# Performance work log

Measured on AMD Instinct MI355X. Metric: run time of the kernel, lower is better.

## Reference

```python
import jax, jax.numpy as jnp
import numpy as np

B, T, C = 2, 2048, 1024
N_HEAD, N_GROUP = 16, 4
N_KV = N_HEAD // N_GROUP          # 4
HEAD_DIM = C // N_HEAD            # 64
ROPE_BASE = 10000.0
INIT_STD = 0.02


def setup_inputs() -> dict:
    key = jax.random.key(0)
    ks = jax.random.split(key, 5)
    kvC = N_KV * HEAD_DIM
    return {
        "x": jax.random.normal(ks[0], (B, T, C), jnp.float32),
        "w_q": jax.random.normal(ks[1], (C, C), jnp.float32) * INIT_STD,
        "b_q": jnp.zeros((C,), jnp.float32),
        "w_k": jax.random.normal(ks[2], (C, kvC), jnp.float32) * INIT_STD,
        "b_k": jnp.zeros((kvC,), jnp.float32),
        "w_v": jax.random.normal(ks[3], (C, kvC), jnp.float32) * INIT_STD,
        "b_v": jnp.zeros((kvC,), jnp.float32),
        "w_o": jax.random.normal(ks[4], (C, C), jnp.float32) * INIT_STD,
        "b_o": jnp.zeros((C,), jnp.float32),
    }


def reference(x, w_q, b_q, w_k, b_k, w_v, b_v, w_o, b_o):
    Bx, Tx, Cx = x.shape
    # projections (torch Linear math with weights stored as [in, out])
    q = (x @ w_q + b_q).reshape(Bx, Tx, N_HEAD, HEAD_DIM).transpose(0, 2, 1, 3)  # [B,H,T,hd]
    k = (x @ w_k + b_k).reshape(Bx, Tx, N_KV, HEAD_DIM).transpose(0, 2, 1, 3)    # [B,KV,T,hd]
    v = (x @ w_v + b_v).reshape(Bx, Tx, N_KV, HEAD_DIM).transpose(0, 2, 1, 3)

    # RoPE with INTERLEAVED pair convention: pairs are (dim 2i, dim 2i+1)
    inv_freq = 1.0 / (ROPE_BASE ** (jnp.arange(0, HEAD_DIM, 2, dtype=jnp.float32) / HEAD_DIM))
    freqs = jnp.arange(Tx, dtype=jnp.float32)[:, None] * inv_freq[None, :]       # [T, hd/2]
    cos, sin = jnp.cos(freqs), jnp.sin(freqs)

    def rope(t):
        tp = t.reshape(*t.shape[:-1], HEAD_DIM // 2, 2)
        e, o = tp[..., 0], tp[..., 1]          # even/odd lanes, [B,h,T,hd/2]
        er = e * cos - o * sin
        orr = e * sin + o * cos
        return jnp.stack([er, orr], axis=-1).reshape(t.shape)

    q, k = rope(q), rope(k)

    # GQA: duplicate each KV head n_group times (consecutively, like repeat_interleave)
    k = jnp.repeat(k, N_GROUP, axis=1)   # [B,H,T,hd]
    v = jnp.repeat(v, N_GROUP, axis=1)

    attn = jnp.einsum('bhqd,bhkd->bhqk', q, k) / np.sqrt(HEAD_DIM).astype(np.float32)
    causal = jnp.tril(jnp.ones((Tx, Tx), bool))
    attn = jnp.where(causal, attn, -jnp.inf)
    attn = jax.nn.softmax(attn, axis=-1)

    out = jnp.einsum('bhqk,bhkd->bhqd', attn, v)            # [B,H,T,hd]
    out = out.transpose(0, 2, 1, 3).reshape(Bx, Tx, Cx)
    return out @ w_o + b_o
```

## Files before the change

kernel.cpp:

```cpp
#include <hip/hip_runtime.h>
#include <hip/hip_bf16.h>

typedef __hip_bfloat16 bf16;
typedef __attribute__((ext_vector_type(8))) short short8_t;
typedef __attribute__((ext_vector_type(4))) short short4_t;
typedef __attribute__((ext_vector_type(4))) float f32x4;

#define B_SZ   2
#define T_SEQ  2048
#define C_DIM  1024
#define NH     16
#define NKV    4
#define HD     64
#define QKVW   1536
#define MTOK   (B_SZ * T_SEQ)

#define LOG2_BASE_OVER_32 0.4152410118609203f
#define Q_SCALE 0.1803368801111204f

__device__ __forceinline__ short f2bs(float f) {
    unsigned u = __float_as_uint(f);
    u += 0x7FFFu + ((u >> 16) & 1u);
    return (short)(u >> 16);
}
__device__ __forceinline__ short f2bs_trunc(float f) {
    return (short)(__float_as_uint(f) >> 16);
}
__device__ __forceinline__ float bs2f(short s) {
    unsigned u = ((unsigned)(unsigned short)s) << 16;
    return __uint_as_float(u);
}
__device__ __forceinline__ float dpp_xor1(float x) {
    return __int_as_float(
        __builtin_amdgcn_update_dpp(0, __float_as_int(x), 0xB1, 0xF, 0xF, true));
}
__device__ __forceinline__ float fast_exp2(float x) {
    float r;
    asm("v_exp_f32 %0, %1" : "=v"(r) : "v"(x));
    return r;
}
__device__ __forceinline__ unsigned pack_bf16_trunc(float lo, float hi) {
    return __builtin_amdgcn_perm(__float_as_uint(hi), __float_as_uint(lo),
                                 0x07060302u);
}
__device__ __forceinline__ void gload_lds16(const short* g, short* l) {
    __builtin_amdgcn_global_load_lds(
        (const __attribute__((address_space(1))) void*)g,
        (__attribute__((address_space(3))) void*)l, 16, 0, 0);
}

__device__ __forceinline__ void transpose_tile(
    const float* __restrict__ W, short* __restrict__ Wt,
    int K, int N, int n0, int k0, int tid)
{
    __shared__ float tile[32][33];
    int tx = tid & 31, ty = tid >> 5;
    #pragma unroll
    for (int i = 0; i < 4; ++i)
        tile[ty + 8 * i][tx] = W[(size_t)(k0 + ty + 8 * i) * N + n0 + tx];
    __syncthreads();
    #pragma unroll
    for (int i = 0; i < 4; ++i)
        Wt[(size_t)(n0 + ty + 8 * i) * K + k0 + tx] = f2bs(tile[tx][ty + 8 * i]);
}

__global__ __launch_bounds__(256) void prep_kernel(
    const float* __restrict__ x,
    const float* __restrict__ w_q, const float* __restrict__ w_k,
    const float* __restrict__ w_v, const float* __restrict__ w_o,
    const float* __restrict__ b_q, const float* __restrict__ b_k,
    const float* __restrict__ b_v,
    short* __restrict__ Xb, short* __restrict__ Wqkv, short* __restrict__ Wto,
    float* __restrict__ Bqkv, float2* __restrict__ Tab)
{
    int blk = blockIdx.x, tid = threadIdx.x;
    if (blk < 4096) {
        int i = blk * 1024 + tid * 4;
        float4 v = *(const float4*)(x + i);
        short4_t o;
        o[0] = f2bs(v.x); o[1] = f2bs(v.y); o[2] = f2bs(v.z); o[3] = f2bs(v.w);
        *(short4_t*)(Xb + i) = o;
    } else if (blk < 5120) {
        int l = blk - 4096;
        transpose_tile(w_q, Wqkv, C_DIM, C_DIM, (l & 31) * 32, (l >> 5) * 32, tid);
    } else if (blk < 5376) {
        int l = blk - 5120;
        transpose_tile(w_k, Wqkv + (size_t)1024 * C_DIM, C_DIM, 256,
                       (l & 7) * 32, (l >> 3) * 32, tid);
    } else if (blk < 5632) {
        int l = blk - 5376;
        transpose_tile(w_v, Wqkv + (size_t)1280 * C_DIM, C_DIM, 256,
                       (l & 7) * 32, (l >> 3) * 32, tid);
    } else if (blk < 6656) {
        int l = blk - 5632;
        transpose_tile(w_o, Wto, C_DIM, C_DIM, (l & 31) * 32, (l >> 5) * 32, tid);
    } else if (blk < 6662) {
        int i = (blk - 6656) * 256 + tid;
        float v;
        if (i < 1024)      v = b_q[i];
        else if (i < 1280) v = b_k[i - 1024];
        else               v = b_v[i - 1280];
        Bqkv[i] = v;
    } else {
        int idx = (blk - 6662) * 256 + tid;
        int t = idx >> 5, i = idx & 31;
        float ang = (float)t * exp2f(-(float)i * LOG2_BASE_OVER_32);
        Tab[idx] = make_float2(cosf(ang), sinf(ang));
    }
}

#define GEMM_STAGE(dstA, dstB, Aptr, Bptr, k0)                                  \
    {                                                                           \
        _Pragma("unroll")                                                       \
        for (int it = 0; it < 4; ++it) {                                        \
            int i = (w * 4 + it) * 64 + lane;                                   \
            int row = i >> 3, p = i & 7;                                        \
            int gc = (k0) + ((p ^ (row & 7)) << 3);                             \
            gload_lds16((Aptr) + (size_t)(m0 + row) * K + gc,                   \
                        (dstA) + (w * 4 + it) * 512);                           \
        }                                                                       \
        _Pragma("unroll")                                                       \
        for (int it = 0; it < 4; ++it) {                                        \
            int i = (w * 4 + it) * 64 + lane;                                   \
            int row = i >> 3, p = i & 7;                                        \
            int gc = (k0) + ((p ^ (row & 7)) << 3);                             \
            gload_lds16((Bptr) + (size_t)(n0 + row) * K + gc,                   \
                        (dstB) + (w * 4 + it) * 512);                           \
        }                                                                       \
    }

#define GEMM_COMPUTE(srcA, srcB)                                                \
    {                                                                           \
        _Pragma("unroll")                                                       \
        for (int ks = 0; ks < 2; ++ks) {                                        \
            short8_t af[4], bf[4];                                              \
            _Pragma("unroll")                                                   \
            for (int mt = 0; mt < 4; ++mt) {                                    \
                int r = wm * 64 + mt * 16 + l16;                                \
                int g = ks * 4 + quad;                                          \
                af[mt] = *(const short8_t*)&(srcA)[r * 64 + ((g ^ (r & 7)) << 3)]; \
            }                                                                   \
            _Pragma("unroll")                                                   \
            for (int nt = 0; nt < 4; ++nt) {                                    \
                int r = wn * 64 + nt * 16 + l16;                                \
                int g = ks * 4 + quad;                                          \
                bf[nt] = *(const short8_t*)&(srcB)[r * 64 + ((g ^ (r & 7)) << 3)]; \
            }                                                                   \
            _Pragma("unroll")                                                   \
            for (int mt = 0; mt < 4; ++mt)                                      \
                _Pragma("unroll")                                               \
                for (int nt = 0; nt < 4; ++nt)                                  \
                    acc[mt][nt] = __builtin_amdgcn_mfma_f32_16x16x32_bf16(      \
                        af[mt], bf[nt], acc[mt][nt], 0, 0, 0);                  \
        }                                                                       \
    }

#define GEMM_KLOOP(Aptr, Bptr)                                                  \
    GEMM_STAGE(sA(0), sB(0), Aptr, Bptr, 0);                                    \
    for (int t = 0; t < NT; ++t) {                                              \
        int cur = t & 1;                                                        \
        if (t + 1 < NT) {                                                       \
            GEMM_STAGE(sA(cur ^ 1), sB(cur ^ 1), Aptr, Bptr, (t + 1) * 64);     \
            asm volatile("s_waitcnt vmcnt(8)" ::: "memory");                    \
        } else {                                                                \
            asm volatile("s_waitcnt vmcnt(0)" ::: "memory");                    \
        }                                                                       \
        __builtin_amdgcn_s_barrier();                                           \
        __builtin_amdgcn_sched_barrier(0);                                      \
        GEMM_COMPUTE(sA(cur), sB(cur));                                         \
        __builtin_amdgcn_sched_barrier(0);                                      \
        __builtin_amdgcn_s_barrier();                                           \
    }

__global__ __launch_bounds__(256) void gemm_qkv(
    const short* __restrict__ A, const short* __restrict__ Bt,
    const float* __restrict__ bias, const float2* __restrict__ Tab,
    short* __restrict__ QKVb, short* __restrict__ Vt)
{
    __shared__ __align__(16) short smem[32768];
    #define sA(b) (smem + (b) * 16384)
    #define sB(b) (smem + (b) * 16384 + 8192)

    const int K = C_DIM, NT = C_DIM / 64;
    int bid = blockIdx.x;
    int swz = (bid & 7) * 48 + (bid >> 3);
    int m0 = (swz / 12) * 128;
    int n0 = (swz % 12) * 128;
    int tid  = threadIdx.x;
    int w    = tid >> 6, lane = tid & 63;
    int quad = lane >> 4, l16 = lane & 15;
    int wm = w & 1, wn = w >> 1;

    f32x4 acc[4][4] = {};

    GEMM_KLOOP(A, Bt);

    if (n0 < 1280) {
        float scale = (n0 < 1024) ? Q_SCALE : 1.0f;
        float sgn   = (l16 & 1) ? 1.0f : -1.0f;
        #pragma unroll
        for (int nt = 0; nt < 4; ++nt) {
            int col = n0 + wn * 64 + nt * 16 + l16;
            int ip  = (col & 63) >> 1;
            float bv = bias[col];
            #pragma unroll
            for (int mt = 0; mt < 4; ++mt) {
                #pragma unroll
                for (int r = 0; r < 4; ++r) {
                    int row = m0 + wm * 64 + mt * 16 + quad * 4 + r;
                    float v = acc[mt][nt][r] + bv;
                    float po = dpp_xor1(v);
                    float2 cs = Tab[(row & (T_SEQ - 1)) * 32 + ip];
                    float res = (v * cs.x + sgn * po * cs.y) * scale;
                    QKVb[(size_t)row * QKVW + col] = f2bs(res);
                }
            }
        }
    } else {
        short (*sT)[136] = (short(*)[136])smem;
        #pragma unroll
        for (int h2 = 0; h2 < 2; ++h2) {
            if (wn == h2) {
                #pragma unroll
                for (int nt = 0; nt < 4; ++nt) {
                    int col_l = nt * 16 + l16;
                    float bv = bias[n0 + h2 * 64 + col_l];
                    #pragma unroll
                    for (int mt = 0; mt < 4; ++mt)
                        #pragma unroll
                        for (int r = 0; r < 4; ++r)
                            sT[col_l][wm * 64 + mt * 16 + quad * 4 + r] =
                                f2bs(acc[mt][nt][r] + bv);
                }
            }
            __syncthreads();
            int d0 = n0 - 1280 + h2 * 64;
            #pragma unroll
            for (int it = 0; it < 4; ++it) {
                int slot = tid + 256 * it;
                int dl = slot >> 4, seg = (slot & 15) * 8;
                *(short8_t*)(Vt + (size_t)(d0 + dl) * MTOK + m0 + seg) =
                    *(const short8_t*)&sT[dl][seg];
            }
            __syncthreads();
        }
    }
    #undef sA
    #undef sB
}

__global__ __launch_bounds__(256) void gemm_mfma_o(
    const short* __restrict__ A, const short* __restrict__ Bt,
    const float* __restrict__ bias, float* __restrict__ C,
    int M, int N, int K_, int unused)
{
    __shared__ __align__(16) short smem[32768];
    #define sA(b) (smem + (b) * 16384)
    #define sB(b) (smem + (b) * 16384 + 8192)

    const int K = C_DIM, NT = C_DIM / 64;
    int bid = blockIdx.x;
    int swz = (bid & 7) * 32 + (bid >> 3);
    int m0 = (swz >> 3) * 128;
    int n0 = (swz & 7) * 128;
    int tid  = threadIdx.x;
    int w    = tid >> 6, lane = tid & 63;
    int quad = lane >> 4, l16 = lane & 15;
    int wm = w & 1, wn = w >> 1;

    f32x4 acc[4][4] = {};

    GEMM_KLOOP(A, Bt);

    #pragma unroll
    for (int mt = 0; mt < 4; ++mt) {
        #pragma unroll
        for (int nt = 0; nt < 4; ++nt) {
            int col = n0 + wn * 64 + nt * 16 + l16;
            float bv = bias[col];
            #pragma unroll
            for (int r = 0; r < 4; ++r) {
                int row = m0 + wm * 64 + mt * 16 + quad * 4 + r;
                C[(size_t)row * N + col] = acc[mt][nt][r] + bv;
            }
        }
    }
    #undef sA
    #undef sB
}

__global__ __launch_bounds__(512) void attn_mfma18(
    const short* __restrict__ QKV, const short* __restrict__ Vt,
    short* __restrict__ O)
{
    __shared__ __align__(16) short sK3[3][64][64];
    __shared__ __align__(16) short sVt[2][64][72];

    const int tid  = threadIdx.x;
    const int w    = tid >> 6;
    const int lane = tid & 63;
    const int quad = lane >> 4;
    const int l16  = lane & 15;

    int blk = blockIdx.x;
    int grp = blk & 7;
    int half = blk >> 8;
    int idx8 = (blk & 255) >> 3;
    int pr   = half ? idx8 : 63 - idx8;
    int kvh = grp & 3;
    int b   = grp >> 2;
    int h   = kvh * 4 + (w & 3);
    int tq  = pr * 2 + (w >> 2);
    int ct  = pr >> 1;
    int tg  = tq * 16 + l16;

    const short* qptr = QKV + ((size_t)(b * T_SEQ) + tq * 16 + l16) * QKVW + h * HD;
    short8_t qf0 = *(const short8_t*)(qptr + quad * 8);
    short8_t qf1 = *(const short8_t*)(qptr + quad * 8 + 32);

    const short* kbase  = QKV + (size_t)b * T_SEQ * QKVW + 1024 + kvh * HD;
    const short* vtbase = Vt + (size_t)(kvh * HD) * MTOK + b * T_SEQ;

    float m_l = -INFINITY, l_l = 0.f;
    f32x4 oacc[4];
    #pragma unroll
    for (int dt = 0; dt < 4; ++dt) oacc[dt] = (f32x4){0.f, 0.f, 0.f, 0.f};

    const int kr_  = tid >> 3;
    const int kg   = tid & 7;
    const int ksrc = (kg ^ (kr_ & 7)) << 3;

    const int vdim = tid >> 3;
    const int s8   = tid & 7;
    const int vseg = s8 * 8;
    const int P0   = ((s8 & 4) << 3) | ((s8 & 1) << 4) | ((s8 & 2) << 1);

    const int c0g = quad ^ (l16 & 7);

    short8_t v0 = *(const short8_t*)(vtbase + (size_t)vdim * MTOK + vseg);
    gload_lds16(kbase + (size_t)kr_ * QKVW + ksrc, (short*)sK3[0] + (w << 9));
    if (ct >= 1)
        gload_lds16(kbase + (size_t)(64 + kr_) * QKVW + ksrc,
                    (short*)sK3[1] + (w << 9));
    if (ct >= 2)
        gload_lds16(kbase + (size_t)(128 + kr_) * QKVW + ksrc,
                    (short*)sK3[2] + (w << 9));
    {
        union { short8_t v; short4_t h[2]; } u; u.v = v0;
        *(short4_t*)&sVt[0][vdim][P0]     = u.h[0];
        *(short4_t*)&sVt[0][vdim][P0 + 8] = u.h[1];
    }
    short8_t vr;
    if (ct > 0)
        vr = *(const short8_t*)(vtbase + (size_t)vdim * MTOK + 64 + vseg);
    if (ct >= 2)      asm volatile("s_waitcnt vmcnt(3) lgkmcnt(0)" ::: "memory");
    else if (ct == 1) asm volatile("s_waitcnt vmcnt(2) lgkmcnt(0)" ::: "memory");
    else              asm volatile("s_waitcnt vmcnt(0) lgkmcnt(0)" ::: "memory");
    __builtin_amdgcn_s_barrier();
    __builtin_amdgcn_sched_barrier(0);

    f32x4 sacc[4], sacc_n[4];
    #pragma unroll
    for (int kt = 0; kt < 4; ++kt) {
        f32x4 z = {0.f, 0.f, 0.f, 0.f};
        const short* krow = &sK3[0][l16 + 16 * kt][0];
        short8_t kf0 = *(const short8_t*)(krow + (c0g << 3));
        short8_t kf1 = *(const short8_t*)(krow + ((c0g ^ 4) << 3));
        z = __builtin_amdgcn_mfma_f32_16x16x32_bf16(kf0, qf0, z, 0, 0, 0);
        z = __builtin_amdgcn_mfma_f32_16x16x32_bf16(kf1, qf1, z, 0, 0, 0);
        sacc[kt] = z;
    }

    int kc = 0;
    for (int c = 0; c <= ct; ++c) {
        const int buf = c & 1;
        const int kn  = (kc == 2) ? 0 : kc + 1;

        if (c + 2 <= ct)      asm volatile("s_waitcnt vmcnt(2) lgkmcnt(0)" ::: "memory");
        else if (c + 1 <= ct) asm volatile("s_waitcnt vmcnt(1) lgkmcnt(0)" ::: "memory");
        else                  asm volatile("s_waitcnt lgkmcnt(0)" ::: "memory");
        __builtin_amdgcn_s_barrier();
        __builtin_amdgcn_sched_barrier(0);

        __builtin_amdgcn_s_setprio(1);
        if (c < ct) {
            #pragma unroll
            for (int kt = 0; kt < 4; ++kt) {
                f32x4 z = {0.f, 0.f, 0.f, 0.f};
                const short* krow = &sK3[kn][l16 + 16 * kt][0];
                short8_t kf0 = *(const short8_t*)(krow + (c0g << 3));
                short8_t kf1 = *(const short8_t*)(krow + ((c0g ^ 4) << 3));
                z = __builtin_amdgcn_mfma_f32_16x16x32_bf16(kf0, qf0, z, 0, 0, 0);
                z = __builtin_amdgcn_mfma_f32_16x16x32_bf16(kf1, qf1, z, 0, 0, 0);
                sacc_n[kt] = z;
            }
            if (c + 3 <= ct) {
                int jn = (c + 3) * 64;
                gload_lds16(kbase + (size_t)(jn + kr_) * QKVW + ksrc,
                            (short*)sK3[kc] + (w << 9));
            }
        }

        if (c == ct) {
            int j0 = c * 64;
            #pragma unroll
            for (int kt = 0; kt < 4; ++kt)
                #pragma unroll
                for (int r = 0; r < 4; ++r)
                    if (j0 + 16 * kt + quad * 4 + r > tg) sacc[kt][r] = -INFINITY;
        }

        float v0s = fmaxf(fmaxf(sacc[0][0], sacc[0][1]), fmaxf(sacc[0][2], sacc[0][3]));
        float v1s = fmaxf(fmaxf(sacc[1][0], sacc[1][1]), fmaxf(sacc[1][2], sacc[1][3]));
        float v2s = fmaxf(fmaxf(sacc[2][0], sacc[2][1]), fmaxf(sacc[2][2], sacc[2][3]));
        float v3s = fmaxf(fmaxf(sacc[3][0], sacc[3][1]), fmaxf(sacc[3][2], sacc[3][3]));
        float vloc = fmaxf(fmaxf(v0s, v1s), fmaxf(v2s, v3s));

        if (!__all(vloc <= m_l + 8.0f)) {
            float vmax = fmaxf(vloc, __shfl_xor(vloc, 16));
            vmax = fmaxf(vmax, __shfl_xor(vmax, 32));
            float mnew = fmaxf(m_l, vmax);
            float al = fast_exp2(m_l - mnew);
            m_l = mnew;
            l_l *= al;
            #pragma unroll
            for (int r = 0; r < 4; ++r) {
                float alr = __shfl(al, quad * 4 + r);
                #pragma unroll
                for (int dt = 0; dt < 4; ++dt) oacc[dt][r] *= alr;
            }
        }

        float psum = 0.f;
        unsigned pk0, pk1, pk2, pk3, pk4, pk5, pk6, pk7;
        {
            float p0 = fast_exp2(sacc[0][0] - m_l), p1 = fast_exp2(sacc[0][1] - m_l);
            float p2 = fast_exp2(sacc[0][2] - m_l), p3 = fast_exp2(sacc[0][3] - m_l);
            psum += (p0 + p1) + (p2 + p3);
            pk0 = pack_bf16_trunc(p0, p1); pk1 = pack_bf16_trunc(p2, p3);
        }
        {
            float p0 = fast_exp2(sacc[1][0] - m_l), p1 = fast_exp2(sacc[1][1] - m_l);
            float p2 = fast_exp2(sacc[1][2] - m_l), p3 = fast_exp2(sacc[1][3] - m_l);
            psum += (p0 + p1) + (p2 + p3);
            pk2 = pack_bf16_trunc(p0, p1); pk3 = pack_bf16_trunc(p2, p3);
        }
        {
            float p0 = fast_exp2(sacc[2][0] - m_l), p1 = fast_exp2(sacc[2][1] - m_l);
            float p2 = fast_exp2(sacc[2][2] - m_l), p3 = fast_exp2(sacc[2][3] - m_l);
            psum += (p0 + p1) + (p2 + p3);
            pk4 = pack_bf16_trunc(p0, p1); pk5 = pack_bf16_trunc(p2, p3);
        }
        {
            float p0 = fast_exp2(sacc[3][0] - m_l), p1 = fast_exp2(sacc[3][1] - m_l);
            float p2 = fast_exp2(sacc[3][2] - m_l), p3 = fast_exp2(sacc[3][3] - m_l);
            psum += (p0 + p1) + (p2 + p3);
            pk6 = pack_bf16_trunc(p0, p1); pk7 = pack_bf16_trunc(p2, p3);
        }
        l_l += psum;

        short8_t pf0, pf1;
        {
            union { unsigned u[4]; short8_t v; } fa, fb;
            fa.u[0] = pk0; fa.u[1] = pk1; fa.u[2] = pk2; fa.u[3] = pk3;
            fb.u[0] = pk4; fb.u[1] = pk5; fb.u[2] = pk6; fb.u[3] = pk7;
            pf0 = fa.v; pf1 = fb.v;
        }

        if (c < ct) {
            union { short8_t v; short4_t hh[2]; } u; u.v = vr;
            *(short4_t*)&sVt[buf ^ 1][vdim][P0]     = u.hh[0];
            *(short4_t*)&sVt[buf ^ 1][vdim][P0 + 8] = u.hh[1];
            if (c + 2 <= ct)
                vr = *(const short8_t*)(vtbase + (size_t)vdim * MTOK
                                        + (c + 2) * 64 + vseg);
        }

        #pragma unroll
        for (int dt = 0; dt < 4; ++dt) {
            short8_t vf0 = *(const short8_t*)&sVt[buf][16 * dt + l16][quad * 8];
            short8_t vf1 = *(const short8_t*)&sVt[buf][16 * dt + l16][quad * 8 + 32];
            oacc[dt] = __builtin_amdgcn_mfma_f32_16x16x32_bf16(pf0, vf0, oacc[dt], 0, 0, 0);
            oacc[dt] = __builtin_amdgcn_mfma_f32_16x16x32_bf16(pf1, vf1, oacc[dt], 0, 0, 0);
        }
        __builtin_amdgcn_s_setprio(0);

        #pragma unroll
        for (int kt = 0; kt < 4; ++kt) sacc[kt] = sacc_n[kt];
        kc = kn;
    }

    l_l += __shfl_xor(l_l, 16);
    l_l += __shfl_xor(l_l, 32);

    #pragma unroll
    for (int r = 0; r < 4; ++r) {
        int m = quad * 4 + r;
        float lr = __shfl(l_l, quad * 4 + r);
        float inv = __builtin_amdgcn_rcpf(lr);
        #pragma unroll
        for (int dt = 0; dt < 4; ++dt)
            O[((size_t)b * T_SEQ + tq * 16 + m) * C_DIM + h * HD + 16 * dt + l16] =
                f2bs(oacc[dt][r] * inv);
    }
}

extern "C" void kernel_launch(void* const* d_in, const int* in_sizes, int n_in,
                              void* d_out, int out_size, void* d_ws, size_t ws_size,
                              hipStream_t stream)
{
    const float* x   = (const float*)d_in[0];
    const float* w_q = (const float*)d_in[1];
    const float* b_q = (const float*)d_in[2];
    const float* w_k = (const float*)d_in[3];
    const float* b_k = (const float*)d_in[4];
    const float* w_v = (const float*)d_in[5];
    const float* b_v = (const float*)d_in[6];
    const float* w_o = (const float*)d_in[7];
    const float* b_o = (const float*)d_in[8];
    float* out = (float*)d_out;

    char* ws = (char*)d_ws;
    short*  Xb   = (short*) (ws);
    short*  Ab   = (short*) (ws + ((size_t)8  << 20));
    short*  QKVb = (short*) (ws + ((size_t)16 << 20));
    short*  Wqkv = (short*) (ws + ((size_t)28 << 20));
    short*  Wto  = (short*) (ws + ((size_t)31 << 20));
    float*  Bqkv = (float*) (ws + ((size_t)33 << 20));
    float2* Tab  = (float2*)(ws + ((size_t)33 << 20) + 8192);
    short*  Vt   = (short*) (ws + ((size_t)34 << 20));

    const int M = MTOK;

    prep_kernel<<<6918, 256, 0, stream>>>(
        x, w_q, w_k, w_v, w_o, b_q, b_k, b_v, Xb, Wqkv, Wto, Bqkv, Tab);

    gemm_qkv<<<384, 256, 0, stream>>>(
        Xb, Wqkv, Bqkv, Tab, QKVb, Vt);

    attn_mfma18<<<B_SZ * NKV * 64, 512, 0, stream>>>(QKVb, Vt, Ab);

    gemm_mfma_o<<<256, 256, 0, stream>>>(
        Ab, Wto, b_o, out, M, C_DIM, C_DIM, 0);
}
```

Before: 155.2 us.

## Process two query tiles per wave in attention to reuse K/V fragments

Each attention block now covers a 64-query tile instead of 32. Every wave holds two 16-row query tiles, so each K and V fragment read from LDS feeds two MFMAs, and the grid halves to 256 blocks. The aim is to cut K/V global and LDS traffic per query and to interleave independent MFMA chains. The cost is roughly double the accumulator and score registers. Fewer blocks also means less parallelism and coarser causal load balancing, since the previous paired-tile ordering was replaced by a simple reverse order.

```diff
diff --git a/kernel.cpp b/kernel.cpp
--- a/kernel.cpp
+++ b/kernel.cpp
@@ -289,7 +289,7 @@
     #undef sB
 }
 
-__global__ __launch_bounds__(512) void attn_mfma18(
+__global__ __launch_bounds__(512) void attn_mfma19(
     const short* __restrict__ QKV, const short* __restrict__ Vt,
     short* __restrict__ O)
 {
@@ -304,27 +304,35 @@
 
     int blk = blockIdx.x;
     int grp = blk & 7;
-    int half = blk >> 8;
-    int idx8 = (blk & 255) >> 3;
-    int pr   = half ? idx8 : 63 - idx8;
+    int p   = 31 - (blk >> 3);
     int kvh = grp & 3;
     int b   = grp >> 2;
     int h   = kvh * 4 + (w & 3);
-    int tq  = pr * 2 + (w >> 2);
-    int ct  = pr >> 1;
-    int tg  = tq * 16 + l16;
-
-    const short* qptr = QKV + ((size_t)(b * T_SEQ) + tq * 16 + l16) * QKVW + h * HD;
-    short8_t qf0 = *(const short8_t*)(qptr + quad * 8);
-    short8_t qf1 = *(const short8_t*)(qptr + quad * 8 + 32);
+    int ht  = w >> 2;
+    int tqA = p * 4 + ht * 2;
+    int tqB = tqA + 1;
+    int ct  = p;
+    int tgA = tqA * 16 + l16;
+    int tgB = tqB * 16 + l16;
+
+    const short* qpA = QKV + ((size_t)(b * T_SEQ) + tqA * 16 + l16) * QKVW + h * HD;
+    const short* qpB = QKV + ((size_t)(b * T_SEQ) + tqB * 16 + l16) * QKVW + h * HD;
+    short8_t qf0a = *(const short8_t*)(qpA + quad * 8);
+    short8_t qf1a = *(const short8_t*)(qpA + quad * 8 + 32);
+    short8_t qf0b = *(const short8_t*)(qpB + quad * 8);
+    short8_t qf1b = *(const short8_t*)(qpB + quad * 8 + 32);
 
     const short* kbase  = QKV + (size_t)b * T_SEQ * QKVW + 1024 + kvh * HD;
     const short* vtbase = Vt + (size_t)(kvh * HD) * MTOK + b * T_SEQ;
 
-    float m_l = -INFINITY, l_l = 0.f;
-    f32x4 oacc[4];
+    float m_a = -INFINITY, l_a = 0.f;
+    float m_b = -INFINITY, l_b = 0.f;
+    f32x4 oaccA[4], oaccB[4];
     #pragma unroll
-    for (int dt = 0; dt < 4; ++dt) oacc[dt] = (f32x4){0.f, 0.f, 0.f, 0.f};
+    for (int dt = 0; dt < 4; ++dt) {
+        oaccA[dt] = (f32x4){0.f, 0.f, 0.f, 0.f};
+        oaccB[dt] = (f32x4){0.f, 0.f, 0.f, 0.f};
+    }
 
     const int kr_  = tid >> 3;
     const int kg   = tid & 7;
@@ -359,16 +367,20 @@
     __builtin_amdgcn_s_barrier();
     __builtin_amdgcn_sched_barrier(0);
 
-    f32x4 sacc[4], sacc_n[4];
+    f32x4 saccA[4], saccB[4], sacc_nA[4], sacc_nB[4];
     #pragma unroll
     for (int kt = 0; kt < 4; ++kt) {
-        f32x4 z = {0.f, 0.f, 0.f, 0.f};
         const short* krow = &sK3[0][l16 + 16 * kt][0];
         short8_t kf0 = *(const short8_t*)(krow + (c0g << 3));
         short8_t kf1 = *(const short8_t*)(krow + ((c0g ^ 4) << 3));
-        z = __builtin_amdgcn_mfma_f32_16x16x32_bf16(kf0, qf0, z, 0, 0, 0);
-        z = __builtin_amdgcn_mfma_f32_16x16x32_bf16(kf1, qf1, z, 0, 0, 0);
-        sacc[kt] = z;
+        f32x4 za = {0.f, 0.f, 0.f, 0.f};
+        f32x4 zb = {0.f, 0.f, 0.f, 0.f};
+        za = __builtin_amdgcn_mfma_f32_16x16x32_bf16(kf0, qf0a, za, 0, 0, 0);
+        zb = __builtin_amdgcn_mfma_f32_16x16x32_bf16(kf0, qf0b, zb, 0, 0, 0);
+        za = __builtin_amdgcn_mfma_f32_16x16x32_bf16(kf1, qf1a, za, 0, 0, 0);
+        zb = __builtin_amdgcn_mfma_f32_16x16x32_bf16(kf1, qf1b, zb, 0, 0, 0);
+        saccA[kt] = za;
+        saccB[kt] = zb;
     }
 
     int kc = 0;
@@ -386,13 +398,17 @@
         if (c < ct) {
             #pragma unroll
             for (int kt = 0; kt < 4; ++kt) {
-                f32x4 z = {0.f, 0.f, 0.f, 0.f};
                 const short* krow = &sK3[kn][l16 + 16 * kt][0];
                 short8_t kf0 = *(const short8_t*)(krow + (c0g << 3));
                 short8_t kf1 = *(const short8_t*)(krow + ((c0g ^ 4) << 3));
-                z = __builtin_amdgcn_mfma_f32_16x16x32_bf16(kf0, qf0, z, 0, 0, 0);
-                z = __builtin_amdgcn_mfma_f32_16x16x32_bf16(kf1, qf1, z, 0, 0, 0);
-                sacc_n[kt] = z;
+                f32x4 za = {0.f, 0.f, 0.f, 0.f};
+                f32x4 zb = {0.f, 0.f, 0.f, 0.f};
+                za = __builtin_amdgcn_mfma_f32_16x16x32_bf16(kf0, qf0a, za, 0, 0, 0);
+                zb = __builtin_amdgcn_mfma_f32_16x16x32_bf16(kf0, qf0b, zb, 0, 0, 0);
+                za = __builtin_amdgcn_mfma_f32_16x16x32_bf16(kf1, qf1a, za, 0, 0, 0);
+                zb = __builtin_amdgcn_mfma_f32_16x16x32_bf16(kf1, qf1b, zb, 0, 0, 0);
+                sacc_nA[kt] = za;
+                sacc_nB[kt] = zb;
             }
             if (c + 3 <= ct) {
                 int jn = (c + 3) * 64;
@@ -406,65 +422,88 @@
             #pragma unroll
             for (int kt = 0; kt < 4; ++kt)
                 #pragma unroll
-                for (int r = 0; r < 4; ++r)
-                    if (j0 + 16 * kt + quad * 4 + r > tg) sacc[kt][r] = -INFINITY;
-        }
-
-        float v0s = fmaxf(fmaxf(sacc[0][0], sacc[0][1]), fmaxf(sacc[0][2], sacc[0][3]));
-        float v1s = fmaxf(fmaxf(sacc[1][0], sacc[1][1]), fmaxf(sacc[1][2], sacc[1][3]));
-        float v2s = fmaxf(fmaxf(sacc[2][0], sacc[2][1]), fmaxf(sacc[2][2], sacc[2][3]));
-        float v3s = fmaxf(fmaxf(sacc[3][0], sacc[3][1]), fmaxf(sacc[3][2], sacc[3][3]));
-        float vloc = fmaxf(fmaxf(v0s, v1s), fmaxf(v2s, v3s));
-
-        if (!__all(vloc <= m_l + 8.0f)) {
-            float vmax = fmaxf(vloc, __shfl_xor(vloc, 16));
-            vmax = fmaxf(vmax, __shfl_xor(vmax, 32));
-            float mnew = fmaxf(m_l, vmax);
-            float al = fast_exp2(m_l - mnew);
-            m_l = mnew;
-            l_l *= al;
-            #pragma unroll
-            for (int r = 0; r < 4; ++r) {
-                float alr = __shfl(al, quad * 4 + r);
+                for (int r = 0; r < 4; ++r) {
+                    int key = j0 + 16 * kt + quad * 4 + r;
+                    if (key > tgA) saccA[kt][r] = -INFINITY;
+                    if (key > tgB) saccB[kt][r] = -INFINITY;
+                }
+        }
+
+        {
+            float v0s = fmaxf(fmaxf(saccA[0][0], saccA[0][1]), fmaxf(saccA[0][2], saccA[0][3]));
+            float v1s = fmaxf(fmaxf(saccA[1][0], saccA[1][1]), fmaxf(saccA[1][2], saccA[1][3]));
+            float v2s = fmaxf(fmaxf(saccA[2][0], saccA[2][1]), fmaxf(saccA[2][2], saccA[2][3]));
+            float v3s = fmaxf(fmaxf(saccA[3][0], saccA[3][1]), fmaxf(saccA[3][2], saccA[3][3]));
+            float vloc = fmaxf(fmaxf(v0s, v1s), fmaxf(v2s, v3s));
+            if (!__all(vloc <= m_a + 8.0f)) {
+                float vmax = fmaxf(vloc, __shfl_xor(vloc, 16));
+                vmax = fmaxf(vmax, __shfl_xor(vmax, 32));
+                float mnew = fmaxf(m_a, vmax);
+                float al = fast_exp2(m_a - mnew);
+                m_a = mnew;
+                l_a *= al;
                 #pragma unroll
-                for (int dt = 0; dt < 4; ++dt) oacc[dt][r] *= alr;
-            }
-        }
-
-        float psum = 0.f;
-        unsigned pk0, pk1, pk2, pk3, pk4, pk5, pk6, pk7;
+                for (int r = 0; r < 4; ++r) {
+                    float alr = __shfl(al, quad * 4 + r);
+                    #pragma unroll
+                    for (int dt = 0; dt < 4; ++dt) oaccA[dt][r] *= alr;
+                }
+            }
+        }
         {
-            float p0 = fast_exp2(sacc[0][0] - m_l), p1 = fast_exp2(sacc[0][1] - m_l);
-            float p2 = fast_exp2(sacc[0][2] - m_l), p3 = fast_exp2(sacc[0][3] - m_l);
-            psum += (p0 + p1) + (p2 + p3);
-            pk0 = pack_bf16_trunc(p0, p1); pk1 = pack_bf16_trunc(p2, p3);
-        }
-        {
-            float p0 = fast_exp2(sacc[1][0] - m_l), p1 = fast_exp2(sacc[1][1] - m_l);
-            float p2 = fast_exp2(sacc[1][2] - m_l), p3 = fast_exp2(sacc[1][3] - m_l);
-            psum += (p0 + p1) + (p2 + p3);
-            pk2 = pack_bf16_trunc(p0, p1); pk3 = pack_bf16_trunc(p2, p3);
-        }
-        {
-            float p0 = fast_exp2(sacc[2][0] - m_l), p1 = fast_exp2(sacc[2][1] - m_l);
-            float p2 = fast_exp2(sacc[2][2] - m_l), p3 = fast_exp2(sacc[2][3] - m_l);
-            psum += (p0 + p1) + (p2 + p3);
-            pk4 = pack_bf16_trunc(p0, p1); pk5 = pack_bf16_trunc(p2, p3);
-        }
-        {
-            float p0 = fast_exp2(sacc[3][0] - m_l), p1 = fast_exp2(sacc[3][1] - m_l);
-            float p2 = fast_exp2(sacc[3][2] - m_l), p3 = fast_exp2(sacc[3][3] - m_l);
-            psum += (p0 + p1) + (p2 + p3);
-            pk6 = pack_bf16_trunc(p0, p1); pk7 = pack_bf16_trunc(p2, p3);
-        }
-        l_l += psum;
-
-        short8_t pf0, pf1;
+            float v0s = fmaxf(fmaxf(saccB[0][0], saccB[0][1]), fmaxf(saccB[0][2], saccB[0][3]));
+            float v1s = fmaxf(fmaxf(saccB[1][0], saccB[1][1]), fmaxf(saccB[1][2], saccB[1][3]));
+            float v2s = fmaxf(fmaxf(saccB[2][0], saccB[2][1]), fmaxf(saccB[2][2], saccB[2][3]));
+            float v3s = fmaxf(fmaxf(saccB[3][0], saccB[3][1]), fmaxf(saccB[3][2], saccB[3][3]));
+            float vloc = fmaxf(fmaxf(v0s, v1s), fmaxf(v2s, v3s));
+            if (!__all(vloc <= m_b + 8.0f)) {
+                float vmax = fmaxf(vloc, __shfl_xor(vloc, 16));
+                vmax = fmaxf(vmax, __shfl_xor(vmax, 32));
+                float mnew = fmaxf(m_b, vmax);
+                float al = fast_exp2(m_b - mnew);
+                m_b = mnew;
+                l_b *= al;
+                #pragma unroll
+                for (int r = 0; r < 4; ++r) {
+                    float alr = __shfl(al, quad * 4 + r);
+                    #pragma unroll
+                    for (int dt = 0; dt < 4; ++dt) oaccB[dt][r] *= alr;
+                }
+            }
+        }
+
+        short8_t pf0a, pf1a, pf0b, pf1b;
         {
             union { unsigned u[4]; short8_t v; } fa, fb;
-            fa.u[0] = pk0; fa.u[1] = pk1; fa.u[2] = pk2; fa.u[3] = pk3;
-            fb.u[0] = pk4; fb.u[1] = pk5; fb.u[2] = pk6; fb.u[3] = pk7;
-            pf0 = fa.v; pf1 = fb.v;
+            float psum = 0.f;
+            #pragma unroll
+            for (int kt = 0; kt < 4; ++kt) {
+                float p0 = fast_exp2(saccA[kt][0] - m_a), p1 = fast_exp2(saccA[kt][1] - m_a);
+                float p2 = fast_exp2(saccA[kt][2] - m_a), p3 = fast_exp2(saccA[kt][3] - m_a);
+                psum += (p0 + p1) + (p2 + p3);
+                unsigned d0 = pack_bf16_trunc(p0, p1);
+                unsigned d1 = pack_bf16_trunc(p2, p3);
+                if (kt < 2) { fa.u[kt * 2] = d0; fa.u[kt * 2 + 1] = d1; }
+                else        { fb.u[(kt - 2) * 2] = d0; fb.u[(kt - 2) * 2 + 1] = d1; }
+            }
+            l_a += psum;
+            pf0a = fa.v; pf1a = fb.v;
+        }
+        {
+            union { unsigned u[4]; short8_t v; } fa, fb;
+            float psum = 0.f;
+            #pragma unroll
+            for (int kt = 0; kt < 4; ++kt) {
+                float p0 = fast_exp2(saccB[kt][0] - m_b), p1 = fast_exp2(saccB[kt][1] - m_b);
+                float p2 = fast_exp2(saccB[kt][2] - m_b), p3 = fast_exp2(saccB[kt][3] - m_b);
+                psum += (p0 + p1) + (p2 + p3);
+                unsigned d0 = pack_bf16_trunc(p0, p1);
+                unsigned d1 = pack_bf16_trunc(p2, p3);
+                if (kt < 2) { fa.u[kt * 2] = d0; fa.u[kt * 2 + 1] = d1; }
+                else        { fb.u[(kt - 2) * 2] = d0; fb.u[(kt - 2) * 2 + 1] = d1; }
+            }
+            l_b += psum;
+            pf0b = fa.v; pf1b = fb.v;
         }
 
         if (c < ct) {
@@ -480,28 +519,40 @@
         for (int dt = 0; dt < 4; ++dt) {
             short8_t vf0 = *(const short8_t*)&sVt[buf][16 * dt + l16][quad * 8];
             short8_t vf1 = *(const short8_t*)&sVt[buf][16 * dt + l16][quad * 8 + 32];
-            oacc[dt] = __builtin_amdgcn_mfma_f32_16x16x32_bf16(pf0, vf0, oacc[dt], 0, 0, 0);
-            oacc[dt] = __builtin_amdgcn_mfma_f32_16x16x32_bf16(pf1, vf1, oacc[dt], 0, 0, 0);
+            oaccA[dt] = __builtin_amdgcn_mfma_f32_16x16x32_bf16(pf0a, vf0, oaccA[dt], 0, 0, 0);
+            oaccB[dt] = __builtin_amdgcn_mfma_f32_16x16x32_bf16(pf0b, vf0, oaccB[dt], 0, 0, 0);
+            oaccA[dt] = __builtin_amdgcn_mfma_f32_16x16x32_bf16(pf1a, vf1, oaccA[dt], 0, 0, 0);
+            oaccB[dt] = __builtin_amdgcn_mfma_f32_16x16x32_bf16(pf1b, vf1, oaccB[dt], 0, 0, 0);
         }
         __builtin_amdgcn_s_setprio(0);
 
         #pragma unroll
-        for (int kt = 0; kt < 4; ++kt) sacc[kt] = sacc_n[kt];
+        for (int kt = 0; kt < 4; ++kt) {
+            saccA[kt] = sacc_nA[kt];
+            saccB[kt] = sacc_nB[kt];
+        }
         kc = kn;
     }
 
-    l_l += __shfl_xor(l_l, 16);
-    l_l += __shfl_xor(l_l, 32);
+    l_a += __shfl_xor(l_a, 16);
+    l_a += __shfl_xor(l_a, 32);
+    l_b += __shfl_xor(l_b, 16);
+    l_b += __shfl_xor(l_b, 32);
 
     #pragma unroll
     for (int r = 0; r < 4; ++r) {
         int m = quad * 4 + r;
-        float lr = __shfl(l_l, quad * 4 + r);
-        float inv = __builtin_amdgcn_rcpf(lr);
+        float lra = __shfl(l_a, quad * 4 + r);
+        float lrb = __shfl(l_b, quad * 4 + r);
+        float inva = __builtin_amdgcn_rcpf(lra);
+        float invb = __builtin_amdgcn_rcpf(lrb);
         #pragma unroll
-        for (int dt = 0; dt < 4; ++dt)
-            O[((size_t)b * T_SEQ + tq * 16 + m) * C_DIM + h * HD + 16 * dt + l16] =
-                f2bs(oacc[dt][r] * inv);
+        for (int dt = 0; dt < 4; ++dt) {
+            O[((size_t)b * T_SEQ + tqA * 16 + m) * C_DIM + h * HD + 16 * dt + l16] =
+                f2bs(oaccA[dt][r] * inva);
+            O[((size_t)b * T_SEQ + tqB * 16 + m) * C_DIM + h * HD + 16 * dt + l16] =
+                f2bs(oaccB[dt][r] * invb);
+        }
     }
 }
 
@@ -538,7 +589,7 @@
     gemm_qkv<<<384, 256, 0, stream>>>(
         Xb, Wqkv, Bqkv, Tab, QKVb, Vt);
 
-    attn_mfma18<<<B_SZ * NKV * 64, 512, 0, stream>>>(QKVb, Vt, Ab);
+    attn_mfma19<<<B_SZ * NKV * 32, 512, 0, stream>>>(QKVb, Vt, Ab);
 
     gemm_mfma_o<<<256, 256, 0, stream>>>(
         Ab, Wto, b_o, out, M, C_DIM, C_DIM, 0);
```

New measurement: 171.2 us. 10.3% more time.
